# Performance work log

Measured on AMD Instinct MI355X. Metric: run time of the kernel, lower is better.

## Reference

```python
import jax, jax.numpy as jnp
import numpy as np

B, CIN, COUT, H, W, K, S, P = 16, 256, 128, 64, 64, 4, 2, 1
PAD = K - 1 - P  # transposed-conv equivalent padding for the lhs-dilated conv


def setup_inputs() -> dict:
    key = jax.random.key(0)
    ks = jax.random.split(key, 13)
    return {
        "x": jax.random.normal(ks[0], (B, CIN, H, W), jnp.float32),
        "feature": jax.random.uniform(ks[1], (B, 4), jnp.float32),
        "weight": jax.random.normal(ks[2], (CIN, COUT, K, K), jnp.float32) * 0.05,
        "t_bayer": jax.random.normal(ks[3], (1, CIN, COUT, K, K), jnp.float32) * 0.05,
        "t_quad": jax.random.normal(ks[4], (1, CIN, COUT, K, K), jnp.float32) * 0.05,
        "t_nano": jax.random.normal(ks[5], (1, CIN, COUT, K, K), jnp.float32) * 0.05,
        "t_qxq": jax.random.normal(ks[6], (1, CIN, COUT, K, K), jnp.float32) * 0.05,
        "m_bayer": jax.random.uniform(ks[7], (1, CIN, COUT, 1, 1), jnp.float32),
        "m_quad": jax.random.uniform(ks[8], (1, CIN, COUT, 1, 1), jnp.float32),
        "m_nano": jax.random.uniform(ks[9], (1, CIN, COUT, 1, 1), jnp.float32),
        "m_qxq": jax.random.uniform(ks[10], (1, CIN, COUT, 1, 1), jnp.float32),
        "bias": jax.random.normal(ks[11], (COUT,), jnp.float32) * 0.05,
        "prelu_a": jnp.full((1,), 0.25, jnp.float32),
    }


def _synth_weights(feature, weight, t_bayer, t_quad, t_nano, t_qxq,
                   m_bayer, m_quad, m_nano, m_qxq):
    # feature: (B,4) softmax attention -> (B,4,1,1,1)
    sa = feature[:, :, None, None, None]
    dyn = (t_bayer * m_bayer * sa[:, 0:1]
           + t_quad * m_quad * sa[:, 1:2]
           + t_nano * m_nano * sa[:, 2:3]
           + t_qxq * m_qxq * sa[:, 3:4])  # (B, CIN, COUT, K, K)
    return weight[None] + dyn  # broadcast base weight over batch


def _deconv_per_sample(xi, wi):
    # xi: (CIN,H,W); wi: (CIN,COUT,K,K) torch conv_transpose layout.
    # conv_transpose == lhs-dilated conv with spatially-flipped, transposed kernel
    kern = jnp.flip(jnp.swapaxes(wi, 0, 1), axis=(-2, -1))  # (COUT,CIN,K,K)
    out = jax.lax.conv_general_dilated(
        xi[None], kern, window_strides=(1, 1),
        padding=[(PAD, PAD), (PAD, PAD)], lhs_dilation=(S, S),
        dimension_numbers=("NCHW", "OIHW", "NCHW"))
    return out[0]  # (COUT, H*S, W*S)


def reference(x, feature, weight, t_bayer, t_quad, t_nano, t_qxq,
              m_bayer, m_quad, m_nano, m_qxq, bias, prelu_a):
    w = _synth_weights(feature, weight, t_bayer, t_quad, t_nano, t_qxq,
                       m_bayer, m_quad, m_nano, m_qxq)
    out = jax.vmap(_deconv_per_sample)(x, w)  # (B, COUT, 128, 128)
    out = out + bias[None, :, None, None]
    # PReLU with single shared slope (torch default init 0.25)
    return jnp.where(out >= 0, out, prelu_a[0] * out)
```

## Files before the change

kernel.cpp:

```cpp
#include <hip/hip_runtime.h>
#include <hip/hip_bf16.h>
#include <cstddef>
#include <cstdint>

#define B_    16
#define CIN_  256
#define COUT_ 128
#define H_    64
#define W_    64
#define OH_   128
#define OW_   128

#define AST   44
#define ACHUNK (128*AST)

typedef __attribute__((ext_vector_type(8))) short bf16x8;
typedef __attribute__((ext_vector_type(4))) float f32x4;

__device__ inline short f2bf(float f) {
    __hip_bfloat16 h = __float2bfloat16(f);
    return *reinterpret_cast<short*>(&h);
}

__device__ inline void async_ld16(const void* g, void* l) {
    typedef const __attribute__((address_space(1))) unsigned int* gp_t;
    typedef __attribute__((address_space(3))) unsigned int* lp_t;
    __builtin_amdgcn_global_load_lds((gp_t)g, (lp_t)l, 16, 0, 0);
}

__device__ inline void synth_body(
    int chunk, int cog8, int tid,
    const float* __restrict__ weight,
    const float* __restrict__ tb, const float* __restrict__ tq,
    const float* __restrict__ tn, const float* __restrict__ tx,
    const float* __restrict__ mb, const float* __restrict__ mq,
    const float* __restrict__ mn, const float* __restrict__ mx,
    const float* __restrict__ feat,
    short* __restrict__ aws,
    short* lbuf )
{
    const int ci_l = tid >> 5;
    const int co_l = (tid >> 2) & 7;
    const int kh   = tid & 3;
    const int base = (chunk*8 + ci_l) * COUT_ + cog8*8 + co_l;

    const float4 w4 = *(const float4*)(weight + (size_t)base*16 + kh*4);
    const float4 b4 = *(const float4*)(tb + (size_t)base*16 + kh*4);
    const float4 q4 = *(const float4*)(tq + (size_t)base*16 + kh*4);
    const float4 n4 = *(const float4*)(tn + (size_t)base*16 + kh*4);
    const float4 x4 = *(const float4*)(tx + (size_t)base*16 + kh*4);
    const float m_b = mb[base], m_q = mq[base];
    const float m_n = mn[base], m_x = mx[base];
    const float* wp = (const float*)&w4;
    const float* bp = (const float*)&b4;
    const float* qp = (const float*)&q4;
    const float* np = (const float*)&n4;
    const float* xp = (const float*)&x4;

    const int r  = (kh+1)&1;
    const int dh = (kh<2) ? 1 : 0;

    for (int b = 0; b < 16; ++b) {
        const float sb = m_b * feat[b*4+0];
        const float sq = m_q * feat[b*4+1];
        const float sn = m_n * feat[b*4+2];
        const float sx = m_x * feat[b*4+3];
        #pragma unroll
        for (int kw = 0; kw < 4; ++kw) {
            int s  = (kw+1)&1;
            int dw = (kw<2) ? 1 : 0;
            float v = wp[kw] + sb*bp[kw] + sq*qp[kw] + sn*np[kw] + sx*xp[kw];
            lbuf[((r*2+s)*8 + co_l)*32 + (dh*2+dw)*8 + ci_l] = f2bf(v);
        }
        __syncthreads();
        if (tid < 128) {
            int cls  = tid >> 5;
            int j    = tid & 31;
            int co_r = j >> 2, t4 = j & 3;
            size_t dst = ((((size_t)(b*4 + cls)*32 + chunk)*128)
                          + cog8*8 + co_r) * AST + t4*8;
            *(int4*)(aws + dst) = *(const int4*)(lbuf + (cls*8 + co_r)*32 + t4*8);
        }
        __syncthreads();
    }
}

__device__ inline void transform_body(
    int ihp, int b, int tid,
    const float* __restrict__ x, short* __restrict__ xt,
    float* xls )
{
    const int4 z4 = {0, 0, 0, 0};

    if (ihp == 0 || ihp == 65) {
        for (int j = tid; j < 2112; j += 256) {
            int c = j / 66, iwp = j - c*66;
            *(int4*)(xt + ((((size_t)b*32 + c)*66 + ihp)*66 + iwp)*8) = z4;
        }
        return;
    }
    if (tid < 64) {
        int c = tid >> 1, iwp = (tid & 1) * 65;
        *(int4*)(xt + ((((size_t)b*32 + c)*66 + ihp)*66 + iwp)*8) = z4;
    }
    const int ih = ihp - 1;
    for (int half = 0; half < 2; ++half) {
        __syncthreads();
        #pragma unroll
        for (int it = 0; it < 8; ++it) {
            int ci_l = it*16 + (tid >> 4);
            int iw4  = (tid & 15) * 4;
            float4 v = *(const float4*)(
                x + (((size_t)b*256 + half*128 + ci_l)*64 + ih)*64 + iw4);
            *(float4*)(xls + ci_l*68 + iw4) = v;
        }
        __syncthreads();
        #pragma unroll
        for (int it2 = 0; it2 < 4; ++it2) {
            int chunk_l = it2*4 + (tid >> 6);
            int chunk   = half*16 + chunk_l;
            int iw      = tid & 63;
            short s8[8];
            #pragma unroll
            for (int j = 0; j < 8; ++j)
                s8[j] = f2bf(xls[(chunk_l*8 + j)*68 + iw]);
            *(int4*)(xt + ((((size_t)b*32 + chunk)*66 + ihp)*66 + (iw+1))*8)
                = *(const int4*)s8;
        }
    }
}

__global__ __launch_bounds__(256) void prep_fused(
    const float* __restrict__ x,
    const float* __restrict__ weight,
    const float* __restrict__ tb, const float* __restrict__ tq,
    const float* __restrict__ tn, const float* __restrict__ tx,
    const float* __restrict__ mb, const float* __restrict__ mq,
    const float* __restrict__ mn, const float* __restrict__ mx,
    const float* __restrict__ feat,
    short* __restrict__ aws, short* __restrict__ xt)
{
    __shared__ __align__(16) char smem[34816];
    const int bid = blockIdx.x;
    const int tid = threadIdx.x;
    if (bid < 1056) {
        int ihp = bid % 66, b = bid / 66;
        transform_body(ihp, b, tid, x, xt, (float*)smem);
    } else {
        int sb = bid - 1056;
        int chunk = sb & 31, cog8 = sb >> 5;
        synth_body(chunk, cog8, tid, weight, tb, tq, tn, tx,
                   mb, mq, mn, mx, feat, aws, (short*)smem);
    }
}

__global__ __launch_bounds__(256) void synth_aws(
    const float* __restrict__ weight,
    const float* __restrict__ tb, const float* __restrict__ tq,
    const float* __restrict__ tn, const float* __restrict__ tx,
    const float* __restrict__ mb, const float* __restrict__ mq,
    const float* __restrict__ mn, const float* __restrict__ mx,
    const float* __restrict__ feat,
    short* __restrict__ aws)
{
    __shared__ __align__(16) short lbuf[4][8][32];
    synth_body(blockIdx.x, blockIdx.y, threadIdx.x, weight, tb, tq, tn, tx,
               mb, mq, mn, mx, feat, aws, &lbuf[0][0][0]);
}

__global__ __launch_bounds__(256) void deconv_mfma2(
    const short* __restrict__ aws, const short* __restrict__ xt,
    const float* __restrict__ bias, const float* __restrict__ prelu_a,
    float* __restrict__ out)
{
    const int tid  = threadIdx.x;
    const int lane = tid & 63;
    const int wv   = tid >> 6;
    const int wm   = wv & 1, wn = wv >> 1;
    const int o    = blockIdx.x;
    const int x8   = o & 7;
    const int l    = o >> 3;
    const int cls  = l & 3;
    const int nt   = (l >> 2) & 31;
    const int b    = 2*x8 + (l >> 7);
    const int a0 = (nt >> 2) * 8, c0 = (nt & 3) * 16;
    const int r = cls >> 1, s = cls & 1;

    __shared__ __align__(16) short als[2][ACHUNK];
    __shared__ __align__(16) short xsb[2][1536];

    const short* gb[4]; int gstep[4], loff[4], isB[4], act[4];
    {
        const size_t awb = (((size_t)b*4 + cls)*32) * ACHUNK;
        #pragma unroll
        for (int i = 0; i < 4; ++i) {
            int t = wv + i*4;
            act[i] = (t < 14);
            if (t < 11) {
                gb[i]    = aws + awb + t*512 + lane*8;
                gstep[i] = ACHUNK;  loff[i] = t*512;  isB[i] = 0;
            } else {
                int j = t - 11;
                int p = j*64 + lane; if (p > 152) p = 152;
                int row = p / 17, col = p - row*17;
                gb[i] = xt + (((size_t)b*32*66 + (a0 + r + row))*66
                              + (c0 + s + col)) * 8;
                gstep[i] = 66*66*8;  loff[i] = j*512;  isB[i] = 1;
            }
        }
    }

    f32x4 acc[4][4];
    #pragma unroll
    for (int mi = 0; mi < 4; ++mi)
        #pragma unroll
        for (int ni = 0; ni < 4; ++ni)
            acc[mi][ni] = (f32x4){0.f, 0.f, 0.f, 0.f};

    const int nlo = lane & 15;
    const int q   = lane >> 4;
    const int dh  = q >> 1, dw = q & 1;

    #pragma unroll
    for (int i = 0; i < 4; ++i)
        if (act[i])
            async_ld16(gb[i], isB[i] ? &xsb[0][loff[i]] : &als[0][loff[i]]);

    for (int c = 0; c < 32; ++c) {
        __syncthreads();
        const int sel = c & 1;
        if (c < 31) {
            const int ps = sel ^ 1;
            #pragma unroll
            for (int i = 0; i < 4; ++i)
                if (act[i])
                    async_ld16(gb[i] + (size_t)(c+1)*gstep[i],
                               isB[i] ? &xsb[ps][loff[i]] : &als[ps][loff[i]]);
        }
        bf16x8 af[4], bfr[4];
        #pragma unroll
        for (int mi = 0; mi < 4; ++mi)
            af[mi] = *(const bf16x8*)(&als[sel][(wm*64 + mi*16 + nlo)*AST + q*8]);
        #pragma unroll
        for (int ni = 0; ni < 4; ++ni) {
            int a_local = wn*4 + ni;
            bfr[ni] = *(const bf16x8*)(&xsb[sel][((a_local + dh)*17 + (nlo + dw))*8]);
        }
        #pragma unroll
        for (int mi = 0; mi < 4; ++mi)
            #pragma unroll
            for (int ni = 0; ni < 4; ++ni)
                acc[mi][ni] = __builtin_amdgcn_mfma_f32_16x16x32_bf16(
                    af[mi], bfr[ni], acc[mi][ni], 0, 0, 0);
    }

    const float pa = prelu_a[0];
    #pragma unroll
    for (int mi = 0; mi < 4; ++mi) {
        #pragma unroll
        for (int reg = 0; reg < 4; ++reg) {
            int co = wm*64 + mi*16 + q*4 + reg;
            float bv = bias[co];
            #pragma unroll
            for (int ni = 0; ni < 4; ++ni) {
                int a_local = wn*4 + ni;
                int oh = 2*(a0 + a_local) + r;
                int ow = 2*(c0 + nlo) + s;
                float v = acc[mi][ni][reg] + bv;
                v = (v >= 0.f) ? v : pa*v;
                out[(((size_t)b*COUT_ + co)*OH_ + oh)*OW_ + ow] = v;
            }
        }
    }
}

__global__ __launch_bounds__(256, 2) void deconv_mfma_gather(
    const float* __restrict__ x,
    const short* __restrict__ aws,
    const float* __restrict__ bias,
    const float* __restrict__ prelu_a,
    float* __restrict__ out)
{
    const int tid  = threadIdx.x;
    const int lane = tid & 63;
    const int wv   = tid >> 6;
    const int wm   = wv & 1, wn = wv >> 1;
    const int nt   = blockIdx.x;
    const int cls  = blockIdx.y;
    const int b    = blockIdx.z;
    const int a0 = (nt >> 2) * 8, c0 = (nt & 3) * 16;
    const int r = cls >> 1, s = cls & 1;

    __shared__ __align__(16) short xs[1280];
    __shared__ __align__(16) short als[ACHUNK];

    int goff[5], gstep[5], gok[5];
    #pragma unroll
    for (int i = 0; i < 5; ++i) {
        int e    = tid + i*256;
        int ci_l = e & 7;
        int rc   = e >> 3;
        int row  = rc / 17;
        int col  = rc - row*17;
        int ih   = a0 - 1 + r + row;
        int iw   = c0 - 1 + s + col;
        int ok   = (rc < 153) && ((unsigned)ih < (unsigned)H_)
                              && ((unsigned)iw < (unsigned)W_);
        goff[i]  = ok ? (((b*CIN_ + ci_l)*H_ + ih)*W_ + iw) : 0;
        gstep[i] = ok ? (8*H_*W_) : 0;
        gok[i]   = ok;
    }
    const size_t aws_base = (((size_t)b*4 + cls)*32) * ACHUNK;

    f32x4 acc[4][4];
    #pragma unroll
    for (int mi = 0; mi < 4; ++mi)
        #pragma unroll
        for (int ni = 0; ni < 4; ++ni)
            acc[mi][ni] = (f32x4){0.f, 0.f, 0.f, 0.f};

    const int nlo = lane & 15;
    const int q   = lane >> 4;
    const int dh  = q >> 1, dw = q & 1;

    for (int chunk = 0; chunk < 32; ++chunk) {
        __syncthreads();
        #pragma unroll
        for (int i = 0; i < 5; ++i) {
            float v = x[goff[i] + chunk*gstep[i]];
            v = gok[i] ? v : 0.0f;
            xs[tid + i*256] = f2bf(v);
        }
        {
            const short* src = aws + aws_base + (size_t)chunk*ACHUNK;
            #pragma unroll
            for (int i = 0; i < 3; ++i) {
                int idx = wv + i*4;
                if (idx < 11)
                    async_ld16(src + idx*512 + lane*8, als + idx*512);
            }
        }
        __syncthreads();
        bf16x8 af[4], bfr[4];
        #pragma unroll
        for (int mi = 0; mi < 4; ++mi)
            af[mi] = *(const bf16x8*)(als + (wm*64 + mi*16 + nlo)*AST + q*8);
        #pragma unroll
        for (int ni = 0; ni < 4; ++ni) {
            int a_local = wn*4 + ni;
            bfr[ni] = *(const bf16x8*)(xs + ((a_local + dh)*17 + (nlo + dw))*8);
        }
        #pragma unroll
        for (int mi = 0; mi < 4; ++mi)
            #pragma unroll
            for (int ni = 0; ni < 4; ++ni)
                acc[mi][ni] = __builtin_amdgcn_mfma_f32_16x16x32_bf16(
                    af[mi], bfr[ni], acc[mi][ni], 0, 0, 0);
    }

    const float pa = prelu_a[0];
    #pragma unroll
    for (int mi = 0; mi < 4; ++mi) {
        #pragma unroll
        for (int reg = 0; reg < 4; ++reg) {
            int co = wm*64 + mi*16 + q*4 + reg;
            float bv = bias[co];
            #pragma unroll
            for (int ni = 0; ni < 4; ++ni) {
                int a_local = wn*4 + ni;
                int oh = 2*(a0 + a_local) + r;
                int ow = 2*(c0 + nlo) + s;
                float v = acc[mi][ni][reg] + bv;
                v = (v >= 0.f) ? v : pa*v;
                out[(((size_t)b*COUT_ + co)*OH_ + oh)*OW_ + ow] = v;
            }
        }
    }
}

__global__ __launch_bounds__(256) void deconv_fallback(
    const float* __restrict__ x,
    const float* __restrict__ weight,
    const float* __restrict__ tb, const float* __restrict__ tq,
    const float* __restrict__ tn, const float* __restrict__ tx,
    const float* __restrict__ mb, const float* __restrict__ mq,
    const float* __restrict__ mn, const float* __restrict__ mx,
    const float* __restrict__ feat,
    const float* __restrict__ bias, const float* __restrict__ prelu_a,
    float* __restrict__ out)
{
    const int tid    = threadIdx.x;
    const int tile   = blockIdx.x;
    const int coT    = blockIdx.y;
    const int b      = blockIdx.z;
    const int tile_h = tile >> 3, tile_w = tile & 7;
    const int a0 = tile_h * 8;
    const int c0 = tile_w * 8;
    const int co0 = coT * 64;

    const int tco = tid & 15;
    const int tpx = tid >> 4;
    const int rr  = tpx >> 2, rc = tpx & 3;

    __shared__ float xsf[4][100];
    __shared__ float wsh[4][16][64];

    float acc[4][4][4];
    #pragma unroll
    for (int i = 0; i < 4; ++i)
        #pragma unroll
        for (int j = 0; j < 4; ++j)
            #pragma unroll
            for (int c = 0; c < 4; ++c) acc[i][j][c] = 0.f;

    float f0 = feat[b*4 + 0], f1 = feat[b*4 + 1];
    float f2 = feat[b*4 + 2], f3 = feat[b*4 + 3];

    for (int chunk = 0; chunk < CIN_ / 4; ++chunk) {
        const int ci0 = chunk * 4;
        __syncthreads();
        for (int e = tid; e < 400; e += 256) {
            int ci_l = e / 100; int rem = e - ci_l * 100;
            int rI = rem / 10;  int cI = rem - rI * 10;
            int ih = a0 - 1 + rI, iw = c0 - 1 + cI;
            float v = 0.f;
            if ((unsigned)ih < (unsigned)H_ && (unsigned)iw < (unsigned)W_)
                v = x[(((size_t)b * CIN_ + ci0 + ci_l) * H_ + ih) * W_ + iw];
            xsf[ci_l][rem] = v;
        }
        #pragma unroll
        for (int k = 0; k < 4; ++k) {
            int g = tid + k * 256;
            int ci_l = g >> 8; int rrem = g & 255;
            int co_l = rrem >> 2; int tg = (rrem & 3) * 4;
            int cico = (ci0 + ci_l) * COUT_ + co0 + co_l;
            int e = cico * 16 + tg;
            float4 w  = *(const float4*)(weight + e);
            float4 vb = *(const float4*)(tb + e);
            float4 vq = *(const float4*)(tq + e);
            float4 vn = *(const float4*)(tn + e);
            float4 vx = *(const float4*)(tx + e);
            float sb = mb[cico] * f0, sq = mq[cico] * f1;
            float sn = mn[cico] * f2, sx = mx[cico] * f3;
            float4 wvv;
            wvv.x = w.x + sb*vb.x + sq*vq.x + sn*vn.x + sx*vx.x;
            wvv.y = w.y + sb*vb.y + sq*vq.y + sn*vn.y + sx*vx.y;
            wvv.z = w.z + sb*vb.z + sq*vq.z + sn*vn.z + sx*vx.z;
            wvv.w = w.w + sb*vb.w + sq*vq.w + sn*vn.w + sx*vx.w;
            wsh[ci_l][tg + 0][co_l] = wvv.x;
            wsh[ci_l][tg + 1][co_l] = wvv.y;
            wsh[ci_l][tg + 2][co_l] = wvv.z;
            wsh[ci_l][tg + 3][co_l] = wvv.w;
        }
        __syncthreads();
        #pragma unroll
        for (int ci_l = 0; ci_l < 4; ++ci_l) {
            float xpv[4][4];
            #pragma unroll
            for (int i = 0; i < 4; ++i)
                #pragma unroll
                for (int j = 0; j < 4; ++j)
                    xpv[i][j] = xsf[ci_l][(rr*2 + i) * 10 + rc*2 + j];
            #pragma unroll
            for (int kh = 0; kh < 4; ++kh) {
                const int rpar = (kh & 1) ? 0 : 1;
                const int offh = (kh == 0) ? 2 : (kh == 3) ? 0 : 1;
                #pragma unroll
                for (int kw = 0; kw < 4; ++kw) {
                    const int spar = (kw & 1) ? 0 : 1;
                    const int offw = (kw == 0) ? 2 : (kw == 3) ? 0 : 1;
                    float4 wvv = *(const float4*)&wsh[ci_l][kh*4 + kw][tco*4];
                    float wr[4] = {wvv.x, wvv.y, wvv.z, wvv.w};
                    #pragma unroll
                    for (int da = 0; da < 2; ++da)
                        #pragma unroll
                        for (int dc = 0; dc < 2; ++dc) {
                            const float xvv = xpv[da + offh][dc + offw];
                            #pragma unroll
                            for (int cc = 0; cc < 4; ++cc)
                                acc[2*da + rpar][2*dc + spar][cc] =
                                    fmaf(wr[cc], xvv, acc[2*da + rpar][2*dc + spar][cc]);
                        }
                }
            }
        }
    }
    const float pa  = prelu_a[0];
    const int oh0 = tile_h * 16 + rr * 4;
    const int ow0 = tile_w * 16 + rc * 4;
    #pragma unroll
    for (int cc = 0; cc < 4; ++cc) {
        const int co = co0 + tco * 4 + cc;
        const float bv = bias[co];
        #pragma unroll
        for (int dr = 0; dr < 4; ++dr)
            #pragma unroll
            for (int dw2 = 0; dw2 < 4; ++dw2) {
                float v = acc[dr][dw2][cc] + bv;
                v = (v >= 0.f) ? v : pa * v;
                out[(((size_t)b * COUT_ + co) * OH_ + (oh0 + dr)) * OW_ + (ow0 + dw2)] = v;
            }
    }
}

extern "C" void kernel_launch(void* const* d_in, const int* in_sizes, int n_in,
                              void* d_out, int out_size, void* d_ws, size_t ws_size,
                              hipStream_t stream) {
    (void)in_sizes; (void)n_in; (void)out_size;
    const float* x      = (const float*)d_in[0];
    const float* feat   = (const float*)d_in[1];
    const float* weight = (const float*)d_in[2];
    const float* tb     = (const float*)d_in[3];
    const float* tq     = (const float*)d_in[4];
    const float* tn     = (const float*)d_in[5];
    const float* tx     = (const float*)d_in[6];
    const float* mb     = (const float*)d_in[7];
    const float* mq     = (const float*)d_in[8];
    const float* mn     = (const float*)d_in[9];
    const float* mx     = (const float*)d_in[10];
    const float* bias   = (const float*)d_in[11];
    const float* prelu  = (const float*)d_in[12];
    float* out = (float*)d_out;

    const size_t aws_sz = (size_t)B_ * 4 * 32 * 128 * AST * sizeof(short);
    const size_t xt_sz  = (size_t)B_ * 32 * 66 * 66 * 8 * sizeof(short);

    if (ws_size >= aws_sz + xt_sz) {
        short* aws = (short*)d_ws;
        short* xt  = (short*)((char*)d_ws + aws_sz);
        prep_fused<<<dim3(1056 + 512), 256, 0, stream>>>(
            x, weight, tb, tq, tn, tx, mb, mq, mn, mx, feat, aws, xt);
        deconv_mfma2<<<dim3(2048), 256, 0, stream>>>(
            aws, xt, bias, prelu, out);
    } else if (ws_size >= aws_sz) {
        short* aws = (short*)d_ws;
        synth_aws<<<dim3(32, 16), 256, 0, stream>>>(
            weight, tb, tq, tn, tx, mb, mq, mn, mx, feat, aws);
        deconv_mfma_gather<<<dim3(32, 4, 16), 256, 0, stream>>>(
            x, aws, bias, prelu, out);
    } else {
        deconv_fallback<<<dim3(64, 2, 16), 256, 0, stream>>>(
            x, weight, tb, tq, tn, tx, mb, mq, mn, mx, feat, bias, prelu, out);
    }
}
```

Measured before the change: 285.8 us.

## Load weight fragments directly from global into registers, drop LDS staging

The MFMA kernel now reads its A operands (the synthesized bf16 weights) straight from global memory into registers. It uses a ping-pong register prefetch of the next K-chunk instead of staging them through double-buffered LDS with async copies. With no LDS bank conflicts to avoid, the row stride padding AST shrinks from 44 to 32, which also shrinks the weight workspace the prep kernel writes and the deconv reads. The trade-off is that each A tile is fetched twice, once per column-wave pair, through the caches. It also raises register pressure and exposes global-load latency to the MFMA loop. The gather fallback gets the same direct-load treatment.

```diff
diff --git a/kernel.cpp b/kernel.cpp
--- a/kernel.cpp
+++ b/kernel.cpp
@@ -11,7 +11,7 @@
 #define OH_   128
 #define OW_   128
 
-#define AST   44
+#define AST   32
 #define ACHUNK (128*AST)
 
 typedef __attribute__((ext_vector_type(8))) short bf16x8;
@@ -168,7 +168,7 @@
                mb, mq, mn, mx, feat, aws, &lbuf[0][0][0]);
 }
 
-__global__ __launch_bounds__(256) void deconv_mfma2(
+__global__ __launch_bounds__(256) void deconv_mfma3(
     const short* __restrict__ aws, const short* __restrict__ xt,
     const float* __restrict__ bias, const float* __restrict__ prelu_a,
     float* __restrict__ out)
@@ -186,72 +186,64 @@
     const int a0 = (nt >> 2) * 8, c0 = (nt & 3) * 16;
     const int r = cls >> 1, s = cls & 1;
 
-    __shared__ __align__(16) short als[2][ACHUNK];
     __shared__ __align__(16) short xsb[2][1536];
-
-    const short* gb[4]; int gstep[4], loff[4], isB[4], act[4];
-    {
-        const size_t awb = (((size_t)b*4 + cls)*32) * ACHUNK;
-        #pragma unroll
-        for (int i = 0; i < 4; ++i) {
-            int t = wv + i*4;
-            act[i] = (t < 14);
-            if (t < 11) {
-                gb[i]    = aws + awb + t*512 + lane*8;
-                gstep[i] = ACHUNK;  loff[i] = t*512;  isB[i] = 0;
-            } else {
-                int j = t - 11;
-                int p = j*64 + lane; if (p > 152) p = 152;
-                int row = p / 17, col = p - row*17;
-                gb[i] = xt + (((size_t)b*32*66 + (a0 + r + row))*66
-                              + (c0 + s + col)) * 8;
-                gstep[i] = 66*66*8;  loff[i] = j*512;  isB[i] = 1;
-            }
-        }
-    }
-
-    f32x4 acc[4][4];
-    #pragma unroll
-    for (int mi = 0; mi < 4; ++mi)
-        #pragma unroll
-        for (int ni = 0; ni < 4; ++ni)
-            acc[mi][ni] = (f32x4){0.f, 0.f, 0.f, 0.f};
 
     const int nlo = lane & 15;
     const int q   = lane >> 4;
     const int dh  = q >> 1, dw = q & 1;
 
-    #pragma unroll
-    for (int i = 0; i < 4; ++i)
-        if (act[i])
-            async_ld16(gb[i], isB[i] ? &xsb[0][loff[i]] : &als[0][loff[i]]);
-
-    for (int c = 0; c < 32; ++c) {
-        __syncthreads();
-        const int sel = c & 1;
+    const size_t awb = (((size_t)b*4 + cls)*32) * ACHUNK;
+    const short* agp = aws + awb + (wm*64 + nlo)*AST + q*8;
+
+    const short* gbB = xt;
+    if (wv < 3) {
+        int p = wv*64 + lane; if (p > 152) p = 152;
+        int row = p / 17, col = p - row*17;
+        gbB = xt + (((size_t)b*32*66 + (a0 + r + row))*66 + (c0 + s + col)) * 8;
+    }
+
+    f32x4 acc[4][4];
+    #pragma unroll
+    for (int mi = 0; mi < 4; ++mi)
+        #pragma unroll
+        for (int ni = 0; ni < 4; ++ni)
+            acc[mi][ni] = (f32x4){0.f, 0.f, 0.f, 0.f};
+
+    bf16x8 afP[4], afQ[4];
+    #pragma unroll
+    for (int mi = 0; mi < 4; ++mi)
+        afP[mi] = *(const bf16x8*)(agp + mi*16*AST);
+    if (wv < 3) async_ld16(gbB, &xsb[0][wv*512]);
+
+    auto step = [&](int c, bf16x8 (&afU)[4], bf16x8 (&afN)[4]) {
+        __syncthreads();
         if (c < 31) {
-            const int ps = sel ^ 1;
-            #pragma unroll
-            for (int i = 0; i < 4; ++i)
-                if (act[i])
-                    async_ld16(gb[i] + (size_t)(c+1)*gstep[i],
-                               isB[i] ? &xsb[ps][loff[i]] : &als[ps][loff[i]]);
-        }
-        bf16x8 af[4], bfr[4];
-        #pragma unroll
-        for (int mi = 0; mi < 4; ++mi)
-            af[mi] = *(const bf16x8*)(&als[sel][(wm*64 + mi*16 + nlo)*AST + q*8]);
+            #pragma unroll
+            for (int mi = 0; mi < 4; ++mi)
+                afN[mi] = *(const bf16x8*)(agp + (size_t)(c+1)*ACHUNK
+                                               + mi*16*AST);
+            if (wv < 3)
+                async_ld16(gbB + (size_t)(c+1)*(66*66*8),
+                           &xsb[(c+1)&1][wv*512]);
+        }
+        bf16x8 bfr[4];
+        const short* xb = &xsb[c&1][0];
         #pragma unroll
         for (int ni = 0; ni < 4; ++ni) {
             int a_local = wn*4 + ni;
-            bfr[ni] = *(const bf16x8*)(&xsb[sel][((a_local + dh)*17 + (nlo + dw))*8]);
+            bfr[ni] = *(const bf16x8*)(xb + ((a_local + dh)*17 + (nlo + dw))*8);
         }
         #pragma unroll
         for (int mi = 0; mi < 4; ++mi)
             #pragma unroll
             for (int ni = 0; ni < 4; ++ni)
                 acc[mi][ni] = __builtin_amdgcn_mfma_f32_16x16x32_bf16(
-                    af[mi], bfr[ni], acc[mi][ni], 0, 0, 0);
+                    afU[mi], bfr[ni], acc[mi][ni], 0, 0, 0);
+    };
+
+    for (int cc = 0; cc < 16; ++cc) {
+        step(2*cc,     afP, afQ);
+        step(2*cc + 1, afQ, afP);
     }
 
     const float pa = prelu_a[0];
@@ -292,7 +284,6 @@
     const int r = cls >> 1, s = cls & 1;
 
     __shared__ __align__(16) short xs[1280];
-    __shared__ __align__(16) short als[ACHUNK];
 
     int goff[5], gstep[5], gok[5];
     #pragma unroll
@@ -310,18 +301,19 @@
         gstep[i] = ok ? (8*H_*W_) : 0;
         gok[i]   = ok;
     }
-    const size_t aws_base = (((size_t)b*4 + cls)*32) * ACHUNK;
-
-    f32x4 acc[4][4];
-    #pragma unroll
-    for (int mi = 0; mi < 4; ++mi)
-        #pragma unroll
-        for (int ni = 0; ni < 4; ++ni)
-            acc[mi][ni] = (f32x4){0.f, 0.f, 0.f, 0.f};
-
     const int nlo = lane & 15;
     const int q   = lane >> 4;
     const int dh  = q >> 1, dw = q & 1;
+
+    const size_t awb = (((size_t)b*4 + cls)*32) * ACHUNK;
+    const short* agp = aws + awb + (wm*64 + nlo)*AST + q*8;
+
+    f32x4 acc[4][4];
+    #pragma unroll
+    for (int mi = 0; mi < 4; ++mi)
+        #pragma unroll
+        for (int ni = 0; ni < 4; ++ni)
+            acc[mi][ni] = (f32x4){0.f, 0.f, 0.f, 0.f};
 
     for (int chunk = 0; chunk < 32; ++chunk) {
         __syncthreads();
@@ -331,20 +323,12 @@
             v = gok[i] ? v : 0.0f;
             xs[tid + i*256] = f2bf(v);
         }
-        {
-            const short* src = aws + aws_base + (size_t)chunk*ACHUNK;
-            #pragma unroll
-            for (int i = 0; i < 3; ++i) {
-                int idx = wv + i*4;
-                if (idx < 11)
-                    async_ld16(src + idx*512 + lane*8, als + idx*512);
-            }
-        }
-        __syncthreads();
-        bf16x8 af[4], bfr[4];
+        bf16x8 af[4];
         #pragma unroll
         for (int mi = 0; mi < 4; ++mi)
-            af[mi] = *(const bf16x8*)(als + (wm*64 + mi*16 + nlo)*AST + q*8);
+            af[mi] = *(const bf16x8*)(agp + (size_t)chunk*ACHUNK + mi*16*AST);
+        __syncthreads();
+        bf16x8 bfr[4];
         #pragma unroll
         for (int ni = 0; ni < 4; ++ni) {
             int a_local = wn*4 + ni;
@@ -530,7 +514,7 @@
         short* xt  = (short*)((char*)d_ws + aws_sz);
         prep_fused<<<dim3(1056 + 512), 256, 0, stream>>>(
             x, weight, tb, tq, tn, tx, mb, mq, mn, mx, feat, aws, xt);
-        deconv_mfma2<<<dim3(2048), 256, 0, stream>>>(
+        deconv_mfma3<<<dim3(2048), 256, 0, stream>>>(
             aws, xt, bias, prelu, out);
     } else if (ws_size >= aws_sz) {
         short* aws = (short*)d_ws;
```

After: 302.5 us. 5.8% more time.

## Double the deconv output tile width to 32 columns and halve grid size

Applied to the files above, without the earlier changes.

The main MFMA deconv kernel now computes a 128x(8x32) output tile per block instead of 8x16, so each block holds 4x8 accumulator fragments and stages a wider 9x33 input halo. That reuses each loaded weight chunk across twice as many output columns and halves the grid to 1024 blocks, cutting redundant weight traffic from global memory into LDS. The cost is higher register pressure under a launch bound of 2 blocks, a larger LDS footprint, and fewer blocks in flight. The synth writer now uses all 256 threads with 8-byte stores, and the fallback gather kernel reads weights straight from global memory instead of through LDS.

```diff
diff --git a/kernel.cpp b/kernel.cpp
--- a/kernel.cpp
+++ b/kernel.cpp
@@ -60,6 +60,10 @@
     const int r  = (kh+1)&1;
     const int dh = (kh<2) ? 1 : 0;
 
+    const int o_cls = tid >> 6;
+    const int o_cor = (tid >> 3) & 7;
+    const int o_e8  = tid & 7;
+
     for (int b = 0; b < 16; ++b) {
         const float sb = m_b * feat[b*4+0];
         const float sq = m_q * feat[b*4+1];
@@ -73,13 +77,11 @@
             lbuf[((r*2+s)*8 + co_l)*32 + (dh*2+dw)*8 + ci_l] = f2bf(v);
         }
         __syncthreads();
-        if (tid < 128) {
-            int cls  = tid >> 5;
-            int j    = tid & 31;
-            int co_r = j >> 2, t4 = j & 3;
-            size_t dst = ((((size_t)(b*4 + cls)*32 + chunk)*128)
-                          + cog8*8 + co_r) * AST + t4*8;
-            *(int4*)(aws + dst) = *(const int4*)(lbuf + (cls*8 + co_r)*32 + t4*8);
+        {
+            size_t row = ((((size_t)(b*4 + o_cls)*32 + chunk)*128)
+                          + cog8*8 + o_cor);
+            *(int2*)(aws + row*AST + o_e8*4) =
+                *(const int2*)(lbuf + (o_cls*8 + o_cor)*32 + o_e8*4);
         }
         __syncthreads();
     }
@@ -168,7 +170,7 @@
                mb, mq, mn, mx, feat, aws, &lbuf[0][0][0]);
 }
 
-__global__ __launch_bounds__(256) void deconv_mfma2(
+__global__ __launch_bounds__(256, 2) void deconv_mfma4(
     const short* __restrict__ aws, const short* __restrict__ xt,
     const float* __restrict__ bias, const float* __restrict__ prelu_a,
     float* __restrict__ out)
@@ -181,28 +183,27 @@
     const int x8   = o & 7;
     const int l    = o >> 3;
     const int cls  = l & 3;
-    const int nt   = (l >> 2) & 31;
-    const int b    = 2*x8 + (l >> 7);
-    const int a0 = (nt >> 2) * 8, c0 = (nt & 3) * 16;
+    const int nt2  = (l >> 2) & 15;
+    const int b    = 2*x8 + (l >> 6);
+    const int a0 = (nt2 >> 1) * 8, c0 = (nt2 & 1) * 32;
     const int r = cls >> 1, s = cls & 1;
 
     __shared__ __align__(16) short als[2][ACHUNK];
-    __shared__ __align__(16) short xsb[2][1536];
-
-    const short* gb[4]; int gstep[4], loff[4], isB[4], act[4];
+    __shared__ __align__(16) short xsb[2][2560];
+
+    const short* gb[4]; size_t gstep[4]; int loff[4], isB[4];
     {
         const size_t awb = (((size_t)b*4 + cls)*32) * ACHUNK;
         #pragma unroll
         for (int i = 0; i < 4; ++i) {
             int t = wv + i*4;
-            act[i] = (t < 14);
             if (t < 11) {
                 gb[i]    = aws + awb + t*512 + lane*8;
                 gstep[i] = ACHUNK;  loff[i] = t*512;  isB[i] = 0;
             } else {
                 int j = t - 11;
-                int p = j*64 + lane; if (p > 152) p = 152;
-                int row = p / 17, col = p - row*17;
+                int p = j*64 + lane; if (p > 296) p = 296;
+                int row = p / 33, col = p - row*33;
                 gb[i] = xt + (((size_t)b*32*66 + (a0 + r + row))*66
                               + (c0 + s + col)) * 8;
                 gstep[i] = 66*66*8;  loff[i] = j*512;  isB[i] = 1;
@@ -210,11 +211,11 @@
         }
     }
 
-    f32x4 acc[4][4];
+    f32x4 acc[4][8];
     #pragma unroll
     for (int mi = 0; mi < 4; ++mi)
         #pragma unroll
-        for (int ni = 0; ni < 4; ++ni)
+        for (int ni = 0; ni < 8; ++ni)
             acc[mi][ni] = (f32x4){0.f, 0.f, 0.f, 0.f};
 
     const int nlo = lane & 15;
@@ -223,8 +224,7 @@
 
     #pragma unroll
     for (int i = 0; i < 4; ++i)
-        if (act[i])
-            async_ld16(gb[i], isB[i] ? &xsb[0][loff[i]] : &als[0][loff[i]]);
+        async_ld16(gb[i], isB[i] ? &xsb[0][loff[i]] : &als[0][loff[i]]);
 
     for (int c = 0; c < 32; ++c) {
         __syncthreads();
@@ -233,23 +233,23 @@
             const int ps = sel ^ 1;
             #pragma unroll
             for (int i = 0; i < 4; ++i)
-                if (act[i])
-                    async_ld16(gb[i] + (size_t)(c+1)*gstep[i],
-                               isB[i] ? &xsb[ps][loff[i]] : &als[ps][loff[i]]);
-        }
-        bf16x8 af[4], bfr[4];
+                async_ld16(gb[i] + (size_t)(c+1)*gstep[i],
+                           isB[i] ? &xsb[ps][loff[i]] : &als[ps][loff[i]]);
+        }
+        bf16x8 af[4], bfr[8];
         #pragma unroll
         for (int mi = 0; mi < 4; ++mi)
             af[mi] = *(const bf16x8*)(&als[sel][(wm*64 + mi*16 + nlo)*AST + q*8]);
         #pragma unroll
-        for (int ni = 0; ni < 4; ++ni) {
-            int a_local = wn*4 + ni;
-            bfr[ni] = *(const bf16x8*)(&xsb[sel][((a_local + dh)*17 + (nlo + dw))*8]);
+        for (int ni = 0; ni < 8; ++ni) {
+            int a_local = wn*4 + (ni & 3);
+            int colx    = nlo + (ni >> 2)*16 + dw;
+            bfr[ni] = *(const bf16x8*)(&xsb[sel][((a_local + dh)*33 + colx)*8]);
         }
         #pragma unroll
         for (int mi = 0; mi < 4; ++mi)
             #pragma unroll
-            for (int ni = 0; ni < 4; ++ni)
+            for (int ni = 0; ni < 8; ++ni)
                 acc[mi][ni] = __builtin_amdgcn_mfma_f32_16x16x32_bf16(
                     af[mi], bfr[ni], acc[mi][ni], 0, 0, 0);
     }
@@ -262,10 +262,11 @@
             int co = wm*64 + mi*16 + q*4 + reg;
             float bv = bias[co];
             #pragma unroll
-            for (int ni = 0; ni < 4; ++ni) {
-                int a_local = wn*4 + ni;
+            for (int ni = 0; ni < 8; ++ni) {
+                int a_local = wn*4 + (ni & 3);
+                int cg      = ni >> 2;
                 int oh = 2*(a0 + a_local) + r;
-                int ow = 2*(c0 + nlo) + s;
+                int ow = 2*(c0 + cg*16 + nlo) + s;
                 float v = acc[mi][ni][reg] + bv;
                 v = (v >= 0.f) ? v : pa*v;
                 out[(((size_t)b*COUT_ + co)*OH_ + oh)*OW_ + ow] = v;
@@ -292,7 +293,6 @@
     const int r = cls >> 1, s = cls & 1;
 
     __shared__ __align__(16) short xs[1280];
-    __shared__ __align__(16) short als[ACHUNK];
 
     int goff[5], gstep[5], gok[5];
     #pragma unroll
@@ -310,18 +310,19 @@
         gstep[i] = ok ? (8*H_*W_) : 0;
         gok[i]   = ok;
     }
-    const size_t aws_base = (((size_t)b*4 + cls)*32) * ACHUNK;
-
-    f32x4 acc[4][4];
-    #pragma unroll
-    for (int mi = 0; mi < 4; ++mi)
-        #pragma unroll
-        for (int ni = 0; ni < 4; ++ni)
-            acc[mi][ni] = (f32x4){0.f, 0.f, 0.f, 0.f};
-
     const int nlo = lane & 15;
     const int q   = lane >> 4;
     const int dh  = q >> 1, dw = q & 1;
+
+    const size_t awb = (((size_t)b*4 + cls)*32) * ACHUNK;
+    const short* agp = aws + awb + (wm*64 + nlo)*AST + q*8;
+
+    f32x4 acc[4][4];
+    #pragma unroll
+    for (int mi = 0; mi < 4; ++mi)
+        #pragma unroll
+        for (int ni = 0; ni < 4; ++ni)
+            acc[mi][ni] = (f32x4){0.f, 0.f, 0.f, 0.f};
 
     for (int chunk = 0; chunk < 32; ++chunk) {
         __syncthreads();
@@ -331,20 +332,17 @@
             v = gok[i] ? v : 0.0f;
             xs[tid + i*256] = f2bf(v);
         }
-        {
-            const short* src = aws + aws_base + (size_t)chunk*ACHUNK;
-            #pragma unroll
-            for (int i = 0; i < 3; ++i) {
-                int idx = wv + i*4;
-                if (idx < 11)
-                    async_ld16(src + idx*512 + lane*8, als + idx*512);
-            }
-        }
-        __syncthreads();
-        bf16x8 af[4], bfr[4];
-        #pragma unroll
-        for (int mi = 0; mi < 4; ++mi)
-            af[mi] = *(const bf16x8*)(als + (wm*64 + mi*16 + nlo)*AST + q*8);
+        bf16x8 af[4];
+        #pragma unroll
+        for (int mi = 0; mi < 4; ++mi) {
+            const short* p = agp + (size_t)chunk*ACHUNK + mi*16*AST;
+            union { int2 h[2]; bf16x8 v; } u;
+            u.h[0] = *(const int2*)p;
+            u.h[1] = *(const int2*)(p + 4);
+            af[mi] = u.v;
+        }
+        __syncthreads();
+        bf16x8 bfr[4];
         #pragma unroll
         for (int ni = 0; ni < 4; ++ni) {
             int a_local = wn*4 + ni;
@@ -530,7 +528,7 @@
         short* xt  = (short*)((char*)d_ws + aws_sz);
         prep_fused<<<dim3(1056 + 512), 256, 0, stream>>>(
             x, weight, tb, tq, tn, tx, mb, mq, mn, mx, feat, aws, xt);
-        deconv_mfma2<<<dim3(2048), 256, 0, stream>>>(
+        deconv_mfma4<<<dim3(1024), 256, 0, stream>>>(
             aws, xt, bias, prelu, out);
     } else if (ws_size >= aws_sz) {
         short* aws = (short*)d_ws;
```

Result: no change. 289.1 us (+1.2%).
